# Optimization experiments

Measured on AMD Instinct MI355X. Metric: run time of the kernel, lower is better.

## Reference

```python
import jax, jax.numpy as jnp
import numpy as np

N_NODES = 20000
N_EDGES = 320000
F = 128            # dim == output_dim
L = 3              # num_layers
N_AGG, N_SCALER = 5, 3
POST_IN = F * (N_AGG * N_SCALER + 1)   # cat([x, scaled_agg])

# deg histogram passed to PNAConv -> avg log-degree constant (PyG: mean of log(bin+1))
_DEG_HIST = np.ones(33, dtype=np.float64)
AVG_LOG = float((np.log(np.arange(33) + 1.0) * _DEG_HIST).sum() / _DEG_HIST.sum())


def _init_linear(k, shape):
    # shape (..., fan_in, fan_out); Kaiming-uniform-ish scale on fan_in
    bound = 1.0 / np.sqrt(shape[-2])
    return jax.random.uniform(k, shape, jnp.float32, -bound, bound)


def setup_inputs() -> dict:
    key = jax.random.key(0)
    ks = jax.random.split(key, 10)
    return {
        "x": jax.random.normal(ks[0], (N_NODES, F), jnp.float32),
        "edge_index": jax.random.randint(ks[1], (2, N_EDGES), 0, N_NODES, jnp.int64),
        "W_pre": _init_linear(ks[2], (L, 2 * F, F)),      # pre_nn Linear(2F->F) per layer
        "b_pre": jnp.zeros((L, F), jnp.float32),
        "W_post": _init_linear(ks[3], (L, POST_IN, F)),   # post_nn Linear(16F->F)
        "b_post": jnp.zeros((L, F), jnp.float32),
        "W_lin": _init_linear(ks[4], (L, F, F)),          # PNAConv.lin Linear(F->F)
        "b_lin": jnp.zeros((L, F), jnp.float32),
        "W_out": _init_linear(ks[5], (F, 1)),             # output_layer
        "b_out": jnp.zeros((1,), jnp.float32),
    }


def reference(x, edge_index, W_pre, b_pre, W_post, b_post, W_lin, b_lin, W_out, b_out):
    n = x.shape[0]
    src, dst = edge_index[0], edge_index[1]  # x_j = x[src], x_i = x[dst]; aggregate onto dst

    # degree-based scalers (graph-fixed)
    cnt = jax.ops.segment_sum(jnp.ones((src.shape[0],), x.dtype), dst, num_segments=n)
    deg = jnp.clip(cnt, 1.0)[:, None]           # PyG clamps deg to >= 1
    log_deg = jnp.log(deg + 1.0)
    amp = log_deg / AVG_LOG                     # amplification scaler
    att = AVG_LOG / log_deg                     # attenuation scaler
    iso = (cnt == 0)[:, None]                   # isolated nodes -> min/max aggregates are 0

    for l in range(W_pre.shape[0]):
        # message: pre_nn(cat([x_i, x_j]))  -> [E, F]
        h = jnp.concatenate([x[dst], x[src]], axis=-1) @ W_pre[l] + b_pre[l]

        s = jax.ops.segment_sum(h, dst, num_segments=n)
        mean = s / deg
        mean_sq = jax.ops.segment_sum(h * h, dst, num_segments=n) / deg
        std = jnp.sqrt(jax.nn.relu(mean_sq - mean * mean) + 1e-5)
        mn = jnp.where(iso, 0.0, jax.ops.segment_min(h, dst, num_segments=n))
        mx = jnp.where(iso, 0.0, jax.ops.segment_max(h, dst, num_segments=n))

        agg = jnp.concatenate([mean, s, std, mn, mx], axis=-1)          # [N, 5F]
        scaled = jnp.concatenate([agg, agg * amp, agg * att], axis=-1)  # [N, 15F]

        out = jnp.concatenate([x, scaled], axis=-1) @ W_post[l] + b_post[l]
        x = jax.nn.relu(out @ W_lin[l] + b_lin[l])

    return jnp.squeeze(x @ W_out + b_out)  # target_dim == 1 -> [N]
```

## Files before the change

### kernel.cpp

```cpp
#include <hip/hip_runtime.h>
#include <math.h>

#define NN 20000
#define NE 320000
#define F 128
#define NLAYER 3
#define MPAD 20032
#define SCAN_NB 79

typedef unsigned int u32;
typedef unsigned short u16;
typedef __attribute__((ext_vector_type(8))) short bf16x8;
typedef __attribute__((ext_vector_type(4))) float f32x4;

__device__ __forceinline__ u16 f2bf(float f) {
    union { float f; u32 u; } x{f};
    u32 r = x.u + 0x7FFFu + ((x.u >> 16) & 1u);
    return (u16)(r >> 16);
}
__device__ __forceinline__ float bflo(u32 u) { return __uint_as_float(u << 16); }
__device__ __forceinline__ float bfhi(u32 u) { return __uint_as_float(u & 0xFFFF0000u); }

__device__ __forceinline__ void gload16(const u16* g, u16* l) {
    __builtin_amdgcn_global_load_lds(
        (const __attribute__((address_space(1))) void*)g,
        (__attribute__((address_space(3))) void*)l, 16, 0, 0);
}


__global__ void hist_kernel(const int* __restrict__ dst, int* __restrict__ cnt, int e) {
    int i = blockIdx.x * blockDim.x + threadIdx.x;
    if (i < e) atomicAdd(&cnt[dst[i]], 1);
}

__global__ void scan_p1(const int* __restrict__ cnt, int* __restrict__ bsum) {
    __shared__ int sh[256];
    int i = blockIdx.x * 256 + threadIdx.x;
    int t = threadIdx.x;
    sh[t] = (i < NN) ? cnt[i] : 0;
    __syncthreads();
#pragma unroll
    for (int d = 128; d > 0; d >>= 1) {
        if (t < d) sh[t] += sh[t + d];
        __syncthreads();
    }
    if (t == 0) bsum[blockIdx.x] = sh[0];
}

__global__ void scan_p2(int* __restrict__ bsum) {
    __shared__ int sh[128];
    int t = threadIdx.x;
    int v = (t < SCAN_NB) ? bsum[t] : 0;
    sh[t] = v;
    __syncthreads();
#pragma unroll
    for (int d = 1; d < 128; d <<= 1) {
        int x = (t >= d) ? sh[t - d] : 0;
        __syncthreads();
        sh[t] += x;
        __syncthreads();
    }
    if (t < SCAN_NB) bsum[t] = sh[t] - v;
}

__global__ void scan_p3(const int* __restrict__ cnt, const int* __restrict__ bsum,
                        int* __restrict__ off, float* __restrict__ amp,
                        float* __restrict__ att, float avg_log) {
    __shared__ int sh[256];
    int i = blockIdx.x * 256 + threadIdx.x;
    int t = threadIdx.x;
    int v = (i < NN) ? cnt[i] : 0;
    sh[t] = v;
    __syncthreads();
#pragma unroll
    for (int d = 1; d < 256; d <<= 1) {
        int x = (t >= d) ? sh[t - d] : 0;
        __syncthreads();
        sh[t] += x;
        __syncthreads();
    }
    if (i < NN) {
        int incl = sh[t] + bsum[blockIdx.x];
        off[i] = incl - v;
        if (i == NN - 1) off[NN] = incl;
        float deg = fmaxf((float)v, 1.0f);
        float ld = logf(deg + 1.0f);
        amp[i] = ld / avg_log;
        att[i] = avg_log / ld;
    }
}

__global__ void scatter_kernel(const int* __restrict__ src, const int* __restrict__ dst,
                               const int* __restrict__ off, int* __restrict__ cur,
                               int* __restrict__ csr, int e) {
    int i = blockIdx.x * blockDim.x + threadIdx.x;
    if (i < e) {
        int d = dst[i];
        int p = atomicAdd(&cur[d], 1);
        csr[off[d] + p] = src[i];
    }
}


#define P0 2560000L
#define P1 (P0 + 3L * 256 * 128)
#define P2 (P1 + 3L * 128 * 128)
#define P3 (P2 + 3L * 2048 * 128)
#define P4 (P3 + 3L * 256)
#define P5 (P4 + 3L * 128)
#define P6 (P5 + 2L * NN)

__global__ void prep_all(const float* __restrict__ x, const float* __restrict__ W_pre,
                         const float* __restrict__ W_lin, const float* __restrict__ W_post,
                         const float* __restrict__ b_pre, const float* __restrict__ b_post,
                         const float* __restrict__ b_lin,
                         u16* __restrict__ xbuf,
                         u16* __restrict__ WpreT, u16* __restrict__ WlinT,
                         u16* __restrict__ Wpostb, float* __restrict__ biaspre,
                         float* __restrict__ bcomb,
                         int* __restrict__ cnt, int* __restrict__ cur) {
    long i = (long)blockIdx.x * 256 + threadIdx.x;
    if (i < P0) {
        xbuf[i] = f2bf(x[i]);
    } else if (i < P1) {
        long j = i - P0;
        int l = j / 32768, t = j % 32768;
        int c = t >> 7, k = t & 127;
        int si = (c < 128) ? (k * 128 + c) : ((k + 128) * 128 + (c - 128));
        WpreT[l * 32768 + t] = f2bf(W_pre[l * 32768 + si]);
    } else if (i < P2) {
        long j = i - P1;
        int l = j / 16384, t = j % 16384;
        int c = t >> 7, k = t & 127;
        WlinT[l * 16384 + t] = f2bf(W_lin[l * 16384 + k * 128 + c]);
    } else if (i < P3) {
        long j = i - P2;
        Wpostb[j] = f2bf(W_post[j]);
    } else if (i < P4) {
        long j = i - P3;
        int l = j / 256, t = j % 256;
        biaspre[l * 256 + t] = (t < 128) ? b_pre[l * 128 + t] : 0.f;
    } else if (i < P5) {
        long j = i - P4;
        int l = j / 128, t = j % 128;
        float s = b_lin[l * 128 + t];
        for (int c = 0; c < 128; ++c) s += b_post[l * 128 + c] * W_lin[l * 16384 + c * 128 + t];
        bcomb[l * 128 + t] = s;
    } else if (i < P6) {
        long j = i - P5;
        if (j < NN) cnt[j] = 0; else cur[j - NN] = 0;
    }
}


#define PROC(u) { float v_; \
    v_ = bflo(u); s0 += v_; q0 = fmaf(v_, v_, q0); mn0 = fminf(mn0, v_); mx0 = fmaxf(mx0, v_); \
    v_ = bfhi(u); s1 += v_; q1 = fmaf(v_, v_, q1); mn1 = fminf(mn1, v_); mx1 = fmaxf(mx1, v_); }

__global__ __launch_bounds__(256) void agg_kernel(
    const u16* __restrict__ preC, const u16* __restrict__ preB,
    const int* __restrict__ off, const int* __restrict__ csr,
    u16* __restrict__ aggb) {
    int node = blockIdx.x;
    int tid = threadIdx.x, w = tid >> 6, lane = tid & 63;
    int o0 = off[node], o1 = off[node + 1];
    int deg = o1 - o0;
    int chunk = (deg + 3) >> 2;
    int b0 = o0 + w * chunk;
    int b1 = min(b0 + chunk, o1);
    const u32* bpl = (const u32*)preB + lane;
    float s0 = 0, s1 = 0, q0 = 0, q1 = 0;
    float mn0 = 1e30f, mn1 = 1e30f, mx0 = -1e30f, mx1 = -1e30f;
    int j = b0;
    for (; j + 4 <= b1; j += 4) {
        int i0 = csr[j], i1 = csr[j + 1], i2 = csr[j + 2], i3 = csr[j + 3];
        u32 u0 = bpl[(size_t)i0 * 64];
        u32 u1 = bpl[(size_t)i1 * 64];
        u32 u2 = bpl[(size_t)i2 * 64];
        u32 u3 = bpl[(size_t)i3 * 64];
        PROC(u0); PROC(u1); PROC(u2); PROC(u3);
    }
    for (; j < b1; ++j) { u32 u = bpl[(size_t)csr[j] * 64]; PROC(u); }

    __shared__ float red[8][256];
    red[0][tid] = s0; red[1][tid] = s1; red[2][tid] = q0; red[3][tid] = q1;
    red[4][tid] = mn0; red[5][tid] = mn1; red[6][tid] = mx0; red[7][tid] = mx1;
    __syncthreads();
    if (w != 0) return;

    s0 = 0; s1 = 0; q0 = 0; q1 = 0;
    mn0 = 1e30f; mn1 = 1e30f; mx0 = -1e30f; mx1 = -1e30f;
#pragma unroll
    for (int ww = 0; ww < 4; ++ww) {
        int sl = ww * 64 + lane;
        s0 += red[0][sl]; s1 += red[1][sl];
        q0 += red[2][sl]; q1 += red[3][sl];
        mn0 = fminf(mn0, red[4][sl]); mn1 = fminf(mn1, red[5][sl]);
        mx0 = fmaxf(mx0, red[6][sl]); mx1 = fmaxf(mx1, red[7][sl]);
    }

    int degi = deg;
    float mean0, mean1, sum0, sum1, std0, std1, lo0, lo1, hi0, hi1;
    if (degi == 0) {
        sum0 = sum1 = 0.f; mean0 = mean1 = 0.f;
        std0 = std1 = sqrtf(1e-5f);
        lo0 = lo1 = hi0 = hi1 = 0.f;
    } else {
        u32 uc = ((const u32*)preC)[(size_t)node * 64 + lane];
        float c0 = bflo(uc), c1 = bfhi(uc), dg = (float)degi;
        sum0 = dg * c0 + s0; mean0 = sum0 / dg;
        sum1 = dg * c1 + s1; mean1 = sum1 / dg;
        float msq0 = c0 * c0 + (2.f * c0 * s0 + q0) / dg;
        float msq1 = c1 * c1 + (2.f * c1 * s1 + q1) / dg;
        std0 = sqrtf(fmaxf(msq0 - mean0 * mean0, 0.f) + 1e-5f);
        std1 = sqrtf(fmaxf(msq1 - mean1 * mean1, 0.f) + 1e-5f);
        lo0 = c0 + mn0; lo1 = c1 + mn1; hi0 = c0 + mx0; hi1 = c1 + mx1;
    }
    u32* cr = (u32*)aggb + (size_t)node * 320 + lane;
    float f0[5] = {mean0, sum0, std0, lo0, hi0};
    float f1[5] = {mean1, sum1, std1, lo1, hi1};
#pragma unroll
    for (int a = 0; a < 5; ++a)
        cr[a * 64] = (u32)f2bf(f0[a]) | ((u32)f2bf(f1[a]) << 16);
}


template <bool BIAS, int MODE, bool SWZ>
__global__ __launch_bounds__(256) void mfma_gemm(
    const u16* __restrict__ A, int lda,
    const u16* __restrict__ Bt, int K,
    const float* __restrict__ bias,
    u16* __restrict__ C, u16* __restrict__ C2, int ldc, int Mreal,
    size_t aS, size_t bS, size_t cS) {
    __shared__ u16 As[64 * 32];
    __shared__ u16 Bs[128 * 32];
    int row0, col0;
    if (SWZ) {
        int g = blockIdx.x;
        int row = (g >> 4) * 8 + (g & 7);
        if (row >= 313) return;
        row0 = row * 64;
        col0 = ((g >> 3) & 1) * 128;
    } else {
        row0 = blockIdx.x * 64;
        col0 = blockIdx.y * 128;
    }
    int z = blockIdx.z;
    A += (size_t)z * aS; Bt += (size_t)z * bS; C += (size_t)z * cS;
    int tid = threadIdx.x;
    int w = tid >> 6, lane = tid & 63;

    int arow = tid >> 2, asl = tid & 3;
    const u16* agp = A + (size_t)(row0 + arow) * lda + ((asl ^ ((arow >> 1) & 3)) << 3);
    u16* alds = As + w * 512;
    int br0 = tid >> 2;
    int br1 = 64 + (tid >> 2);
    const u16* bgp0 = Bt + (size_t)(col0 + br0) * K + (((tid & 3) ^ ((br0 >> 1) & 3)) << 3);
    const u16* bgp1 = Bt + (size_t)(col0 + br1) * K + (((tid & 3) ^ ((br1 >> 1) & 3)) << 3);
    u16* blds0 = Bs + w * 512;
    u16* blds1 = Bs + 2048 + w * 512;

    f32x4 acc[2][4];
#pragma unroll
    for (int m = 0; m < 2; ++m)
#pragma unroll
        for (int n = 0; n < 4; ++n) acc[m][n] = (f32x4){0.f, 0.f, 0.f, 0.f};

    int s = lane >> 4, r = lane & 15;
    int wr = (w >> 1) * 32, wc = (w & 1) * 64;

    for (int k0 = 0; k0 < K; k0 += 32) {
        gload16(agp + k0, alds);
        gload16(bgp0 + k0, blds0);
        gload16(bgp1 + k0, blds1);
        __syncthreads();
        bf16x8 a[2], b[4];
#pragma unroll
        for (int m = 0; m < 2; ++m) {
            int row = wr + m * 16 + r;
            a[m] = *(const bf16x8*)&As[row * 32 + ((s ^ ((row >> 1) & 3)) << 3)];
        }
#pragma unroll
        for (int n = 0; n < 4; ++n) {
            int col = wc + n * 16 + r;
            b[n] = *(const bf16x8*)&Bs[col * 32 + ((s ^ ((col >> 1) & 3)) << 3)];
        }
#pragma unroll
        for (int m = 0; m < 2; ++m)
#pragma unroll
            for (int n = 0; n < 4; ++n)
                acc[m][n] = __builtin_amdgcn_mfma_f32_16x16x32_bf16(a[m], b[n], acc[m][n], 0, 0, 0);
        __syncthreads();
    }

#pragma unroll
    for (int m = 0; m < 2; ++m) {
#pragma unroll
        for (int n = 0; n < 4; ++n) {
            int gcol = col0 + wc + n * 16 + r;
            float bs = BIAS ? bias[gcol] : 0.f;
#pragma unroll
            for (int j = 0; j < 4; ++j) {
                int grow = row0 + wr + m * 16 + s * 4 + j;
                if (grow < Mreal) {
                    u16 h = f2bf(acc[m][n][j] + bs);
                    if (MODE == 0) {
                        C[(size_t)grow * ldc + gcol] = h;
                    } else if (MODE == 2) {
                        if (gcol < 128) C[(size_t)grow * 128 + gcol] = h;
                        else            C2[(size_t)grow * 128 + gcol - 128] = h;
                    } else {
                        size_t idx;
                        if (gcol < 128) idx = (size_t)grow * 768 + gcol;
                        else {
                            int t2 = gcol - 128;
                            int gg = t2 / 640;
                            int ko = 128 + t2 - gg * 640;
                            idx = (size_t)(gg * 128 + grow) * 768 + ko;
                        }
                        C[idx] = h;
                    }
                }
            }
        }
    }
}


__global__ __launch_bounds__(256) void comb2(
    const u16* __restrict__ xbuf,
    const u16* __restrict__ aggb,
    const u16* __restrict__ BtK,
    const float* __restrict__ bias,
    const float* __restrict__ amp, const float* __restrict__ att,
    u16* __restrict__ xout) {
    __shared__ u16 S[3][8192];
    int g = blockIdx.x;
    int row = (g >> 4) * 8 + (g & 7);
    if (row >= 313) return;
    int row0 = row * 64;
    int cb = (g >> 3) & 1;
    int tid = threadIdx.x;
    int w = tid >> 6, lane = tid & 63;
    int r = lane & 15, s4 = lane >> 4;
    int wr = (w >> 1) * 32, wc = (w & 1) * 32;

    int rtA = tid >> 2, qA = tid & 3;
    int koffA = (qA ^ ((rtA >> 1) & 3)) << 3;
    const u16* xA = xbuf + (size_t)(row0 + rtA) * 128 + koffA;
    const u16* gA = aggb + (size_t)(row0 + rtA) * 640 + koffA - 128;
    const u16* bB[3];
#pragma unroll
    for (int p = 1; p < 4; ++p) {
        int lid = tid + 256 * p;
        int rt = lid >> 2, q = lid & 3;
        int rb = rt - 64, gg = rb >> 6, jj = rb & 63;
        int koff = (q ^ ((rt >> 1) & 3)) << 3;
        bB[p - 1] = BtK + (size_t)(gg * 128 + cb * 64 + jj) * 768 + koff;
    }

    f32x4 acc[2][3][2];
#pragma unroll
    for (int m = 0; m < 2; ++m)
#pragma unroll
        for (int gg = 0; gg < 3; ++gg)
#pragma unroll
            for (int n = 0; n < 2; ++n) acc[m][gg][n] = (f32x4){0.f, 0.f, 0.f, 0.f};

    auto STAGE = [&](int t, int b) {
        const u16* a = (t < 4) ? (xA + t * 32) : (gA + t * 32);
        gload16(a, &S[b][(size_t)tid * 8]);
#pragma unroll
        for (int p = 1; p < 4; ++p)
            gload16(bB[p - 1] + t * 32, &S[b][(size_t)(tid + 256 * p) * 8]);
    };

    STAGE(0, 0);
    STAGE(1, 1);
    asm volatile("s_waitcnt vmcnt(4)" ::: "memory");
    __builtin_amdgcn_s_barrier();
    asm volatile("" ::: "memory");

    int buf = 0;
    for (int t = 0; t < 24; ++t) {
        if (t + 2 < 24) STAGE(t + 2, (t + 2) % 3);
        const u16* Sb = S[buf];
        bf16x8 a[2];
#pragma unroll
        for (int m = 0; m < 2; ++m) {
            int rw = wr + m * 16 + r;
            a[m] = *(const bf16x8*)&Sb[rw * 32 + ((s4 ^ ((rw >> 1) & 3)) << 3)];
        }
#pragma unroll
        for (int gg = 0; gg < 3; ++gg) {
            if (gg > 0 && t < 4) continue;
#pragma unroll
            for (int n = 0; n < 2; ++n) {
                int rowb = 64 + gg * 64 + wc + n * 16 + r;
                bf16x8 b = *(const bf16x8*)&Sb[rowb * 32 + ((s4 ^ ((rowb >> 1) & 3)) << 3)];
#pragma unroll
                for (int m = 0; m < 2; ++m)
                    acc[m][gg][n] = __builtin_amdgcn_mfma_f32_16x16x32_bf16(a[m], b, acc[m][gg][n], 0, 0, 0);
            }
        }
        if (t < 23) {
            if (t + 2 < 24) asm volatile("s_waitcnt vmcnt(4)" ::: "memory");
            else            asm volatile("s_waitcnt vmcnt(0)" ::: "memory");
            __builtin_amdgcn_s_barrier();
            asm volatile("" ::: "memory");
        }
        buf = (buf == 2) ? 0 : buf + 1;
    }

    int gcb = cb * 64 + wc;
#pragma unroll
    for (int m = 0; m < 2; ++m)
#pragma unroll
        for (int j = 0; j < 4; ++j) {
            int grow = row0 + wr + m * 16 + s4 * 4 + j;
            if (grow < NN) {
                float av = amp[grow], tv = att[grow];
#pragma unroll
                for (int n = 0; n < 2; ++n) {
                    int gcol = gcb + n * 16 + r;
                    float v = acc[m][0][n][j] + av * acc[m][1][n][j] + tv * acc[m][2][n][j] + bias[gcol];
                    v = fmaxf(v, 0.f);
                    xout[(size_t)grow * F + gcol] = f2bf(v);
                }
            }
        }
}


__global__ void out_kernel(const u16* __restrict__ x, const float* __restrict__ Wout,
                           const float* __restrict__ bout, float* __restrict__ y) {
    int gid = blockIdx.x * blockDim.x + threadIdx.x;
    int wid = gid >> 6, lane = threadIdx.x & 63;
    if (wid >= NN) return;
    u32 u = *(const u32*)&x[(size_t)wid * F + 2 * lane];
    float v = bflo(u) * Wout[2 * lane] + bfhi(u) * Wout[2 * lane + 1];
#pragma unroll
    for (int o = 32; o > 0; o >>= 1) v += __shfl_down(v, o, 64);
    if (lane == 0) y[wid] = v + bout[0];
}


extern "C" void kernel_launch(void* const* d_in, const int* in_sizes, int n_in,
                              void* d_out, int out_size, void* d_ws, size_t ws_size,
                              hipStream_t stream) {
    const float* x_in   = (const float*)d_in[0];
    const int*   ei     = (const int*)d_in[1];
    const float* W_pre  = (const float*)d_in[2];
    const float* b_pre  = (const float*)d_in[3];
    const float* W_post = (const float*)d_in[4];
    const float* b_post = (const float*)d_in[5];
    const float* W_lin  = (const float*)d_in[6];
    const float* b_lin  = (const float*)d_in[7];
    const float* W_out  = (const float*)d_in[8];
    const float* b_out  = (const float*)d_in[9];

    const int* src = ei;
    const int* dst = ei + NE;

    double sl = 0.0;
    for (int i = 0; i < 33; ++i) sl += log((double)(i + 1));
    float avg_log = (float)(sl / 33.0);

    char* ws = (char*)d_ws;
    size_t p = 0;
    auto alloc = [&](size_t bytes) { void* r = ws + p; p += (bytes + 255) & ~(size_t)255; return r; };
    u16*   xbuf    = (u16*)alloc((size_t)MPAD * F * 2);
    u16*   aggb    = (u16*)alloc((size_t)MPAD * 640 * 2);
    u16*   preC    = (u16*)alloc((size_t)MPAD * F * 2);
    u16*   preB    = (u16*)alloc((size_t)MPAD * F * 2);
    u16*   WpreT   = (u16*)alloc((size_t)3 * 256 * 128 * 2);
    u16*   Wpostb  = (u16*)alloc((size_t)3 * 2048 * 128 * 2);
    u16*   WlinT   = (u16*)alloc((size_t)3 * 128 * 128 * 2);
    u16*   BtK     = (u16*)alloc((size_t)3 * 384 * 768 * 2);
    float* biaspre = (float*)alloc((size_t)3 * 256 * 4);
    float* bcomb   = (float*)alloc((size_t)3 * 128 * 4);
    float* amp     = (float*)alloc((size_t)MPAD * 4);
    float* att     = (float*)alloc((size_t)MPAD * 4);
    int*   cnt     = (int*)alloc((size_t)NN * 4);
    int*   offs    = (int*)alloc((size_t)(NN + 1) * 4);
    int*   cur     = (int*)alloc((size_t)NN * 4);
    int*   csr     = (int*)alloc((size_t)NE * 4);
    int*   bsum    = (int*)alloc((size_t)SCAN_NB * 4);
    (void)ws_size;

    prep_all<<<(int)((P6 + 255) / 256), 256, 0, stream>>>(
        x_in, W_pre, W_lin, W_post, b_pre, b_post, b_lin,
        xbuf, WpreT, WlinT, Wpostb, biaspre, bcomb, cnt, cur);

    hist_kernel<<<(NE + 255) / 256, 256, 0, stream>>>(dst, cnt, NE);
    scan_p1<<<SCAN_NB, 256, 0, stream>>>(cnt, bsum);
    scan_p2<<<1, 128, 0, stream>>>(bsum);
    scan_p3<<<SCAN_NB, 256, 0, stream>>>(cnt, bsum, offs, amp, att, avg_log);
    scatter_kernel<<<(NE + 255) / 256, 256, 0, stream>>>(src, dst, offs, cur, csr, NE);

    mfma_gemm<false, 1, false><<<dim3(2, 16, 3), 256, 0, stream>>>(
        WlinT, 128, Wpostb, 128, nullptr, BtK, nullptr, 0, 128,
        16384, 262144, 294912);

    mfma_gemm<true, 2, true><<<640, 256, 0, stream>>>(
        xbuf, F, WpreT, 128, biaspre, preC, preB, 128, MPAD, 0, 0, 0);

    for (int l = 0; l < NLAYER; ++l) {
        agg_kernel<<<NN, 256, 0, stream>>>(preC, preB, offs, csr, aggb);
        comb2<<<640, 256, 0, stream>>>(
            xbuf, aggb, BtK + (size_t)l * 294912, bcomb + (size_t)l * 128,
            amp, att, xbuf);
        if (l < NLAYER - 1) {
            mfma_gemm<true, 2, true><<<640, 256, 0, stream>>>(
                xbuf, F, WpreT + (size_t)(l + 1) * 32768, 128,
                biaspre + (size_t)(l + 1) * 256, preC, preB, 128, MPAD, 0, 0, 0);
        }
    }

    out_kernel<<<5000, 256, 0, stream>>>(xbuf, W_out, b_out, (float*)d_out);
}
```

Baseline: 249.9 us.

## Assign one wavefront per node with grid-stride loop in aggregation kernel

The aggregation kernel previously used a 256-thread block per node, splitting edges across four waves and reducing through shared memory with a barrier. Now each wave owns a whole node and loops over nodes grid-stride over 2048 blocks, with the gather loop unrolled by 8. This removes the LDS reduction, the syncthreads and the idle waves after the reduction, and increases memory-level parallelism per wave. The trade-off is that high-degree nodes become serial within one wave, which can cause load imbalance.

```diff
diff --git a/kernel.cpp b/kernel.cpp
--- a/kernel.cpp
+++ b/kernel.cpp
@@ -161,67 +161,63 @@
     const u16* __restrict__ preC, const u16* __restrict__ preB,
     const int* __restrict__ off, const int* __restrict__ csr,
     u16* __restrict__ aggb) {
-    int node = blockIdx.x;
     int tid = threadIdx.x, w = tid >> 6, lane = tid & 63;
-    int o0 = off[node], o1 = off[node + 1];
-    int deg = o1 - o0;
-    int chunk = (deg + 3) >> 2;
-    int b0 = o0 + w * chunk;
-    int b1 = min(b0 + chunk, o1);
     const u32* bpl = (const u32*)preB + lane;
-    float s0 = 0, s1 = 0, q0 = 0, q1 = 0;
-    float mn0 = 1e30f, mn1 = 1e30f, mx0 = -1e30f, mx1 = -1e30f;
-    int j = b0;
-    for (; j + 4 <= b1; j += 4) {
-        int i0 = csr[j], i1 = csr[j + 1], i2 = csr[j + 2], i3 = csr[j + 3];
-        u32 u0 = bpl[(size_t)i0 * 64];
-        u32 u1 = bpl[(size_t)i1 * 64];
-        u32 u2 = bpl[(size_t)i2 * 64];
-        u32 u3 = bpl[(size_t)i3 * 64];
-        PROC(u0); PROC(u1); PROC(u2); PROC(u3);
-    }
-    for (; j < b1; ++j) { u32 u = bpl[(size_t)csr[j] * 64]; PROC(u); }
-
-    __shared__ float red[8][256];
-    red[0][tid] = s0; red[1][tid] = s1; red[2][tid] = q0; red[3][tid] = q1;
-    red[4][tid] = mn0; red[5][tid] = mn1; red[6][tid] = mx0; red[7][tid] = mx1;
-    __syncthreads();
-    if (w != 0) return;
-
-    s0 = 0; s1 = 0; q0 = 0; q1 = 0;
-    mn0 = 1e30f; mn1 = 1e30f; mx0 = -1e30f; mx1 = -1e30f;
-#pragma unroll
-    for (int ww = 0; ww < 4; ++ww) {
-        int sl = ww * 64 + lane;
-        s0 += red[0][sl]; s1 += red[1][sl];
-        q0 += red[2][sl]; q1 += red[3][sl];
-        mn0 = fminf(mn0, red[4][sl]); mn1 = fminf(mn1, red[5][sl]);
-        mx0 = fmaxf(mx0, red[6][sl]); mx1 = fmaxf(mx1, red[7][sl]);
-    }
-
-    int degi = deg;
-    float mean0, mean1, sum0, sum1, std0, std1, lo0, lo1, hi0, hi1;
-    if (degi == 0) {
-        sum0 = sum1 = 0.f; mean0 = mean1 = 0.f;
-        std0 = std1 = sqrtf(1e-5f);
-        lo0 = lo1 = hi0 = hi1 = 0.f;
-    } else {
-        u32 uc = ((const u32*)preC)[(size_t)node * 64 + lane];
-        float c0 = bflo(uc), c1 = bfhi(uc), dg = (float)degi;
-        sum0 = dg * c0 + s0; mean0 = sum0 / dg;
-        sum1 = dg * c1 + s1; mean1 = sum1 / dg;
-        float msq0 = c0 * c0 + (2.f * c0 * s0 + q0) / dg;
-        float msq1 = c1 * c1 + (2.f * c1 * s1 + q1) / dg;
-        std0 = sqrtf(fmaxf(msq0 - mean0 * mean0, 0.f) + 1e-5f);
-        std1 = sqrtf(fmaxf(msq1 - mean1 * mean1, 0.f) + 1e-5f);
-        lo0 = c0 + mn0; lo1 = c1 + mn1; hi0 = c0 + mx0; hi1 = c1 + mx1;
-    }
-    u32* cr = (u32*)aggb + (size_t)node * 320 + lane;
-    float f0[5] = {mean0, sum0, std0, lo0, hi0};
-    float f1[5] = {mean1, sum1, std1, lo1, hi1};
-#pragma unroll
-    for (int a = 0; a < 5; ++a)
-        cr[a * 64] = (u32)f2bf(f0[a]) | ((u32)f2bf(f1[a]) << 16);
+    int nwaves = gridDim.x * 4;
+    for (int node = blockIdx.x * 4 + w; node < NN; node += nwaves) {
+        int o0 = off[node], o1 = off[node + 1];
+        int deg = o1 - o0;
+        float s0 = 0, s1 = 0, q0 = 0, q1 = 0;
+        float mn0 = 1e30f, mn1 = 1e30f, mx0 = -1e30f, mx1 = -1e30f;
+        int j = o0;
+        for (; j + 8 <= o1; j += 8) {
+            int i0 = csr[j],     i1 = csr[j + 1], i2 = csr[j + 2], i3 = csr[j + 3];
+            int i4 = csr[j + 4], i5 = csr[j + 5], i6 = csr[j + 6], i7 = csr[j + 7];
+            u32 u0 = bpl[(size_t)i0 * 64];
+            u32 u1 = bpl[(size_t)i1 * 64];
+            u32 u2 = bpl[(size_t)i2 * 64];
+            u32 u3 = bpl[(size_t)i3 * 64];
+            u32 u4 = bpl[(size_t)i4 * 64];
+            u32 u5 = bpl[(size_t)i5 * 64];
+            u32 u6 = bpl[(size_t)i6 * 64];
+            u32 u7 = bpl[(size_t)i7 * 64];
+            PROC(u0); PROC(u1); PROC(u2); PROC(u3);
+            PROC(u4); PROC(u5); PROC(u6); PROC(u7);
+        }
+        if (j + 4 <= o1) {
+            int i0 = csr[j], i1 = csr[j + 1], i2 = csr[j + 2], i3 = csr[j + 3];
+            u32 u0 = bpl[(size_t)i0 * 64];
+            u32 u1 = bpl[(size_t)i1 * 64];
+            u32 u2 = bpl[(size_t)i2 * 64];
+            u32 u3 = bpl[(size_t)i3 * 64];
+            PROC(u0); PROC(u1); PROC(u2); PROC(u3);
+            j += 4;
+        }
+        for (; j < o1; ++j) { u32 u = bpl[(size_t)csr[j] * 64]; PROC(u); }
+
+        float mean0, mean1, sum0, sum1, std0, std1, lo0, lo1, hi0, hi1;
+        if (deg == 0) {
+            sum0 = sum1 = 0.f; mean0 = mean1 = 0.f;
+            std0 = std1 = sqrtf(1e-5f);
+            lo0 = lo1 = hi0 = hi1 = 0.f;
+        } else {
+            u32 uc = ((const u32*)preC)[(size_t)node * 64 + lane];
+            float c0 = bflo(uc), c1 = bfhi(uc), dg = (float)deg;
+            sum0 = dg * c0 + s0; mean0 = sum0 / dg;
+            sum1 = dg * c1 + s1; mean1 = sum1 / dg;
+            float msq0 = c0 * c0 + (2.f * c0 * s0 + q0) / dg;
+            float msq1 = c1 * c1 + (2.f * c1 * s1 + q1) / dg;
+            std0 = sqrtf(fmaxf(msq0 - mean0 * mean0, 0.f) + 1e-5f);
+            std1 = sqrtf(fmaxf(msq1 - mean1 * mean1, 0.f) + 1e-5f);
+            lo0 = c0 + mn0; lo1 = c1 + mn1; hi0 = c0 + mx0; hi1 = c1 + mx1;
+        }
+        u32* cr = (u32*)aggb + (size_t)node * 320 + lane;
+        float f0[5] = {mean0, sum0, std0, lo0, hi0};
+        float f1[5] = {mean1, sum1, std1, lo1, hi1};
+#pragma unroll
+        for (int a = 0; a < 5; ++a)
+            cr[a * 64] = (u32)f2bf(f0[a]) | ((u32)f2bf(f1[a]) << 16);
+    }
 }
 
 
@@ -506,7 +502,7 @@
         xbuf, F, WpreT, 128, biaspre, preC, preB, 128, MPAD, 0, 0, 0);
 
     for (int l = 0; l < NLAYER; ++l) {
-        agg_kernel<<<NN, 256, 0, stream>>>(preC, preB, offs, csr, aggb);
+        agg_kernel<<<2048, 256, 0, stream>>>(preC, preB, offs, csr, aggb);
         comb2<<<640, 256, 0, stream>>>(
             xbuf, aggb, BtK + (size_t)l * 294912, bcomb + (size_t)l * 128,
             amp, att, xbuf);
```

New measurement: 222.1 us. 11.1% less time.
